# Optimization experiments

Hardware: AMD Instinct MI355X
Metric: run time of the kernel (lower is better)

## Reference

```python
import jax, jax.numpy as jnp
import numpy as np

NUM_CLASSES = 26
PERCENTILE = 95.0
BIG = jnp.float32(1e10)


def _erode(m):
    # scipy-style binary erosion with cross structuring element, border_value=0
    p = jnp.pad(m, 1, constant_values=False)
    return m & p[:-2, 1:-1] & p[2:, 1:-1] & p[1:-1, :-2] & p[1:-1, 2:]


def _boundary(m):
    return m & ~_erode(m)


def _edt(edge):
    # Exact Euclidean distance transform to nearest True pixel of `edge` [H, W].
    # Two-pass separable formulation (rows then columns), fully vectorized.
    H, W = edge.shape
    r = jnp.arange(H)
    rd2 = ((r[:, None] - r[None, :]) ** 2).astype(jnp.float32)  # [H, H']
    # g[i, j] = min over i' with edge[i', j] of (i - i')^2
    g = jnp.min(jnp.where(edge[None, :, :], rd2[:, :, None], BIG), axis=1)  # [H, W]
    c = jnp.arange(W)
    cd2 = ((c[:, None] - c[None, :]) ** 2).astype(jnp.float32)  # [W', W]
    # dt2[i, j] = min over j' of g[i, j'] + (j' - j)^2
    dt2 = jnp.min(g[:, :, None] + cd2[None, :, :], axis=1)  # [H, W]
    return jnp.sqrt(dt2)


def _pct95(dists, mask):
    # np.percentile(dists[mask], 95) with linear interpolation; nan if mask empty
    n = jnp.sum(mask)
    s = jnp.sort(jnp.where(mask, dists, jnp.inf))
    idx = (PERCENTILE / 100.0) * (n.astype(jnp.float32) - 1.0)
    idx = jnp.maximum(idx, 0.0)
    lo = jnp.floor(idx).astype(jnp.int32)
    hi = jnp.ceil(idx).astype(jnp.int32)
    vlo = s[lo]
    vhi = s[hi]
    val = vlo + (vhi - vlo) * (idx - jnp.floor(idx))
    return jnp.where(n > 0, val, jnp.nan)


def _hd_pair(pl, tl, c):
    # 95th-percentile symmetric Hausdorff between pred/target binary masks of class c
    pm = pl == c
    tm = tl == c
    pe = _boundary(pm)
    te = _boundary(tm)
    dt_t = _edt(te)  # distance to target boundary
    dt_p = _edt(pe)  # distance to pred boundary
    d_pt = _pct95(dt_t.ravel(), pe.ravel())  # pred-edge -> target-edge
    d_tp = _pct95(dt_p.ravel(), te.ravel())  # target-edge -> pred-edge
    return jnp.maximum(d_pt, d_tp)


def setup_inputs() -> dict:
    key = jax.random.key(0)
    k1, k2 = jax.random.split(key)
    predicted = jax.random.normal(k1, (2, NUM_CLASSES, 256, 256), dtype=jnp.float32)
    target = jax.random.normal(k2, (2, NUM_CLASSES, 256, 256), dtype=jnp.float32)
    return {"predicted": predicted, "target": target}


def reference(predicted, target):
    probs = jax.nn.softmax(predicted, axis=1)
    pl = jnp.argmax(probs, axis=1)   # [B, H, W]
    tl = jnp.argmax(target, axis=1)  # [B, H, W]

    def per_class(c):
        hd = jax.vmap(lambda p, t: _hd_pair(p, t, c))(pl, tl)  # [B]
        present = jnp.any(tl == c, axis=(1, 2))                # [B]
        return hd, present

    hds, pres = jax.lax.map(per_class, jnp.arange(NUM_CLASSES))  # [C, B]
    presf = pres.astype(jnp.float32)
    num = jnp.sum(jnp.where(pres, hds, 0.0), axis=0)  # [B]
    den = jnp.sum(presf, axis=0)                      # [B]
    batch_means = num / jnp.maximum(den, 1.0)
    valid = den > 0
    total = jnp.sum(jnp.where(valid, batch_means, 0.0)) / jnp.maximum(
        jnp.sum(valid.astype(jnp.float32)), 1.0)
    return jnp.where(jnp.any(valid), total, jnp.inf)
```

## Files before the change

kernel.cpp:

```cpp
#include <hip/hip_runtime.h>
#include <math.h>

#define HW 65536
#define NC 26
#define NB 2

#define PL_OFF    0
#define TL_OFF    131072
#define CNT_OFF   262144
#define RES_OFF   263424
#define BMP_OFF   264192
#define LISTP_OFF 1116160
#define LISTT_OFF 7931904
#define MINP_OFF  14747648
#define MINT_OFF  28379136

__global__ void k_labels(const float4* __restrict__ pred, const float4* __restrict__ targ,
                         uchar4* __restrict__ pl, uchar4* __restrict__ tl,
                         unsigned int* __restrict__ cnt) {
    int tid = threadIdx.x;
    if (blockIdx.x == 0) {
        for (int i = tid; i < 320; i += 128) cnt[i] = 0;
    }
    int idx = blockIdx.x * 128 + tid;
    if (idx >= (NB * HW / 4)) return;
    int b = idx >> 14, q = idx & 16383;
    const float4* p = pred + ((size_t)b * NC << 14) + q;
    const float4* t = targ + ((size_t)b * NC << 14) + q;
    float4 bp = p[0]; uchar4 ap = {0, 0, 0, 0};
    float4 bt = t[0]; uchar4 at = {0, 0, 0, 0};
#pragma unroll
    for (int c = 1; c < NC; ++c) {
        float4 vp = p[(size_t)c << 14];
        if (vp.x > bp.x) { bp.x = vp.x; ap.x = (unsigned char)c; }
        if (vp.y > bp.y) { bp.y = vp.y; ap.y = (unsigned char)c; }
        if (vp.z > bp.z) { bp.z = vp.z; ap.z = (unsigned char)c; }
        if (vp.w > bp.w) { bp.w = vp.w; ap.w = (unsigned char)c; }
        float4 vt = t[(size_t)c << 14];
        if (vt.x > bt.x) { bt.x = vt.x; at.x = (unsigned char)c; }
        if (vt.y > bt.y) { bt.y = vt.y; at.y = (unsigned char)c; }
        if (vt.z > bt.z) { bt.z = vt.z; at.z = (unsigned char)c; }
        if (vt.w > bt.w) { bt.w = vt.w; at.w = (unsigned char)c; }
    }
    pl[idx] = ap;
    tl[idx] = at;
}

__device__ __forceinline__ bool is_boundary(const unsigned char* __restrict__ L, int hw, int c) {
    int y = hw >> 8, x = hw & 255;
    if (y == 0 || y == 255 || x == 0 || x == 255) return true;
    return (int)L[hw - 256] != c || (int)L[hw + 256] != c ||
           (int)L[hw - 1]   != c || (int)L[hw + 1]   != c;
}

__global__ void k_rowbm(const unsigned char* __restrict__ pl,
                        const unsigned char* __restrict__ tl,
                        unsigned int* __restrict__ bmp,
                        unsigned int* __restrict__ cnt,
                        unsigned short* __restrict__ listP,
                        unsigned short* __restrict__ listT) {
    __shared__ unsigned bm[52][8];
    __shared__ unsigned lh[52];
    __shared__ unsigned lb[52];
    int tid = threadIdx.x;
    int b = blockIdx.x >> 8, y = blockIdx.x & 255;
    for (int i = tid; i < 416; i += 256) ((unsigned*)bm)[i] = 0;
    if (tid < 52) lh[tid] = 0;
    __syncthreads();
    const unsigned char* Lp = pl + (b << 16);
    const unsigned char* Lt = tl + (b << 16);
    int hw = (y << 8) | tid;
    int cp = Lp[hw];
    int ct = Lt[hw];
    bool bnp = is_boundary(Lp, hw, cp);
    bool bnt = is_boundary(Lt, hw, ct);
    unsigned rp = 0, rt = 0;
    if (bnp) {
        atomicOr(&bm[cp][tid >> 5], 1u << (tid & 31));
        rp = atomicAdd(&lh[cp], 1u);
    }
    if (bnt) {
        atomicOr(&bm[26 + ct][tid >> 5], 1u << (tid & 31));
        rt = atomicAdd(&lh[26 + ct], 1u);
    }
    __syncthreads();
    for (int i = tid; i < 416; i += 256) {
        int idx = i >> 3, w = i & 7;
        int m = idx < 26 ? 0 : 1;
        int c = idx < 26 ? idx : idx - 26;
        bmp[(((m * 52 + b * 26 + c) << 8) | y) * 8 + w] = bm[idx][w];
    }
    if (tid < 26)
        lb[tid] = lh[tid] ? atomicAdd(&cnt[208 + b * 26 + tid], lh[tid]) : 0u;
    else if (tid < 52)
        lb[tid] = lh[tid] ? atomicAdd(&cnt[260 + b * 26 + (tid - 26)], lh[tid]) : 0u;
    __syncthreads();
    if (bnp) listP[((unsigned)(b * 26 + cp) << 16) + lb[cp] + rp] = (unsigned short)hw;
    if (bnt) listT[((unsigned)(b * 26 + ct) << 16) + lb[26 + ct] + rt] = (unsigned short)hw;
}

__device__ __forceinline__ int row_dx(const unsigned* sb, const unsigned* rmw,
                                      int r, int xw, int xb) {
    unsigned RM = rmw[r];
    if (!RM) return 999;
    const unsigned* row = sb + r * 9;
    int dxmin = 999;
    unsigned m = row[xw];
    unsigned le = 0xFFFFFFFFu >> (31 - xb);
    unsigned lm = m & le;
    if (lm) dxmin = xb - 31 + __clz(lm);
    unsigned rmm = m & ~le;
    if (rmm) dxmin = min(dxmin, (__ffs(rmm) - 1) - xb);
    unsigned Lm = RM & ((1u << xw) - 1u);
    if (Lm) {
        int w1 = 31 - __clz(Lm);
        unsigned m1 = row[w1];
        dxmin = min(dxmin, xb + ((xw - w1) << 5) - (31 - __clz(m1)));
    }
    unsigned Rm = RM >> (xw + 1);
    if (Rm) {
        int w2 = xw + __ffs(Rm);
        unsigned m2 = row[w2];
        dxmin = min(dxmin, ((w2 - xw) << 5) + (__ffs(m2) - 1) - xb);
    }
    return dxmin;
}

__global__ __launch_bounds__(256) void k_ring(
        const unsigned int* __restrict__ cnt,
        const unsigned int* __restrict__ bmp,
        const unsigned short* __restrict__ listP,
        const unsigned short* __restrict__ listT,
        float* __restrict__ minP, float* __restrict__ minT) {
    int pair = blockIdx.y;
    int dir = blockIdx.z;
    unsigned ns = cnt[(dir ? 260 : 208) + pair];
    unsigned i0 = blockIdx.x * 256u;
    if (i0 >= ns) return;
    unsigned nt = cnt[(dir ? 208 : 260) + pair];
    if (nt == 0) return;
    const unsigned short* src = (dir ? listT : listP) + ((unsigned)pair << 16);
    float* outv = (dir ? minT : minP) + ((unsigned)pair << 16);

    __shared__ unsigned sb[256 * 9];
    __shared__ unsigned rmw[256];
    int tid = threadIdx.x;
    {
        const uint4* g4 = (const uint4*)(bmp + ((unsigned)((dir ? 0 : 52) + pair) << 11));
#pragma unroll
        for (int t = 0; t < 2; ++t) {
            int idx = tid + t * 256;
            uint4 v = g4[idx];
            unsigned* row = sb + (idx >> 1) * 9 + ((idx & 1) << 2);
            row[0] = v.x; row[1] = v.y; row[2] = v.z; row[3] = v.w;
        }
    }
    __syncthreads();
    {
        const unsigned* row = sb + tid * 9;
        unsigned rm = 0;
#pragma unroll
        for (int w = 0; w < 8; ++w) rm |= (row[w] ? 1u : 0u) << w;
        rmw[tid] = rm;
    }
    __syncthreads();

    unsigned stride = gridDim.x * 256u;
    for (unsigned ib = i0; ib < ns; ib += stride) {
        unsigned i = ib + tid;
        if (i >= ns) continue;
        unsigned h = src[i];
        int x = (int)(h & 255u);
        int sy = (int)(h >> 8);
        int xw = x >> 5, xb = x & 31;
        int best = 0x40000000;
        for (int k = 0; k < 256; ++k) {
            int k2 = k * k;
            if (k2 >= best) break;
            int ra = sy - k, rb = sy + k;
            if (ra < 0 && rb > 255) break;
            if (ra >= 0) {
                int dx = row_dx(sb, rmw, ra, xw, xb);
                if (dx < 999) best = min(best, k2 + dx * dx);
            }
            if (k && rb < 256) {
                int dx = row_dx(sb, rmw, rb, xw, xb);
                if (dx < 999) best = min(best, k2 + dx * dx);
            }
        }
        outv[i] = (float)best;
    }
}

__global__ void k_select(const unsigned int* __restrict__ cnt,
                         const float* __restrict__ minP, const float* __restrict__ minT,
                         float* __restrict__ res) {
    int pair = blockIdx.x;
    int dir = blockIdx.y;
    unsigned ns = cnt[(dir ? 260 : 208) + pair];
    unsigned nt = cnt[(dir ? 208 : 260) + pair];
    const float* vals = (dir ? minT : minP) + ((unsigned)pair << 16);
    int tid = threadIdx.x;

    if (ns == 0) { if (tid == 0) res[pair * 2 + dir] = nanf(""); return; }
    if (nt == 0) { if (tid == 0) res[pair * 2 + dir] = sqrtf(1e10f); return; }

    __shared__ unsigned hist[1024];
    __shared__ unsigned f1[128], f2[128];
    __shared__ int s_binlo, s_binhi, s_below_lo, s_below_hi;

    for (int i = tid; i < 1024; i += 256) hist[i] = 0;
    __syncthreads();
    for (unsigned i = tid; i < ns; i += 256) {
        int v = (int)vals[i];
        atomicAdd(&hist[v >> 7], 1u);
    }
    __syncthreads();

    float idxf = 0.95f * ((float)ns - 1.0f);
    if (idxf < 0.f) idxf = 0.f;
    int klo = (int)floorf(idxf);
    int khi = (int)ceilf(idxf);

    if (tid == 0) {
        unsigned cum = 0;
        int binlo = -1, binhi = -1, below_lo = 0, below_hi = 0;
        for (int bkt = 0; bkt < 1024; ++bkt) {
            unsigned h = hist[bkt];
            if (binlo < 0 && cum + h > (unsigned)klo) { binlo = bkt; below_lo = (int)cum; }
            if (binhi < 0 && cum + h > (unsigned)khi) { binhi = bkt; below_hi = (int)cum; }
            cum += h;
            if (binhi >= 0) break;
        }
        s_binlo = binlo; s_binhi = binhi; s_below_lo = below_lo; s_below_hi = below_hi;
    }
    __syncthreads();
    if (tid < 128) { f1[tid] = 0; f2[tid] = 0; }
    __syncthreads();
    int binlo = s_binlo, binhi = s_binhi;
    for (unsigned i = tid; i < ns; i += 256) {
        int v = (int)vals[i];
        int bkt = v >> 7;
        if (bkt == binlo) atomicAdd(&f1[v & 127], 1u);
        if (bkt == binhi && binhi != binlo) atomicAdd(&f2[v & 127], 1u);
    }
    __syncthreads();
    if (tid == 0) {
        int rlo = klo - s_below_lo;
        unsigned cum = 0; int d2lo = binlo << 7, d2hi = binhi << 7;
        for (int j = 0; j < 128; ++j) {
            cum += f1[j];
            if ((int)cum > rlo) { d2lo = (binlo << 7) + j; break; }
        }
        if (binhi == binlo) {
            int rhi = khi - s_below_lo;
            cum = 0;
            for (int j = 0; j < 128; ++j) {
                cum += f1[j];
                if ((int)cum > rhi) { d2hi = (binlo << 7) + j; break; }
            }
        } else {
            int rhi = khi - s_below_hi;
            cum = 0;
            for (int j = 0; j < 128; ++j) {
                cum += f2[j];
                if ((int)cum > rhi) { d2hi = (binhi << 7) + j; break; }
            }
        }
        float vlo = sqrtf((float)d2lo);
        float vhi = sqrtf((float)d2hi);
        float frac = idxf - floorf(idxf);
        res[pair * 2 + dir] = vlo + (vhi - vlo) * frac;
    }
}

__global__ void k_final(const unsigned int* __restrict__ cnt, const float* __restrict__ res,
                        float* __restrict__ out) {
    if (threadIdx.x != 0 || blockIdx.x != 0) return;
    float total = 0.f, nvalid = 0.f;
    bool anyv = false;
    for (int b = 0; b < NB; ++b) {
        float num = 0.f, den = 0.f;
        for (int c = 0; c < NC; ++c) {
            int pair = b * NC + c;
            bool present = cnt[260 + pair] > 0;
            float dpt = res[pair * 2];
            float dtp = res[pair * 2 + 1];
            float hd;
            if (isnan(dpt) || isnan(dtp)) hd = nanf("");
            else hd = fmaxf(dpt, dtp);
            if (present) { num += hd; den += 1.f; }
        }
        float bm = num / fmaxf(den, 1.f);
        if (den > 0.f) { total += bm; nvalid += 1.f; anyv = true; }
    }
    out[0] = anyv ? (total / fmaxf(nvalid, 1.f)) : INFINITY;
}

extern "C" void kernel_launch(void* const* d_in, const int* in_sizes, int n_in,
                              void* d_out, int out_size, void* d_ws, size_t ws_size,
                              hipStream_t stream) {
    const float* pred = (const float*)d_in[0];
    const float* targ = (const float*)d_in[1];
    float* out = (float*)d_out;
    char* ws = (char*)d_ws;

    unsigned char* pl = (unsigned char*)(ws + PL_OFF);
    unsigned char* tl = (unsigned char*)(ws + TL_OFF);
    unsigned int* cnt = (unsigned int*)(ws + CNT_OFF);
    float* res = (float*)(ws + RES_OFF);
    unsigned int* bmp = (unsigned int*)(ws + BMP_OFF);
    unsigned short* listP = (unsigned short*)(ws + LISTP_OFF);
    unsigned short* listT = (unsigned short*)(ws + LISTT_OFF);
    float* minP = (float*)(ws + MINP_OFF);
    float* minT = (float*)(ws + MINT_OFF);

    k_labels<<<256, 128, 0, stream>>>((const float4*)pred, (const float4*)targ,
                                      (uchar4*)pl, (uchar4*)tl, cnt);
    k_rowbm<<<512, 256, 0, stream>>>(pl, tl, bmp, cnt, listP, listT);
    k_ring<<<dim3(12, 52, 2), 256, 0, stream>>>(cnt, bmp, listP, listT, minP, minT);
    k_select<<<dim3(52, 2), 256, 0, stream>>>(cnt, minP, minT, res);
    k_final<<<1, 64, 0, stream>>>(cnt, res, out);
}
```

Measured before the change: 46.66 us.

## Fuse select and final reduction via last-block atomic; shrink ring blocks

Merges the percentile-select and final-averaging kernels into one, where the last block to finish (detected by an atomic counter) computes the final mean. This removes one kernel launch. It also halves the ring kernel's block size while doubling its grid, and stores each row's word-occupancy mask in the padding slot of the shared bitmap row instead of a separate array. The final-reduction path relies on the counter at cnt[313] being zeroed each call by the label kernel and on atomics to make other blocks' writes visible.

Result: slower. 79.24 us (+69.8%).

```diff
diff --git a/kernel.cpp b/kernel.cpp
--- a/kernel.cpp
+++ b/kernel.cpp
@@ -99,11 +99,10 @@
     if (bnt) listT[((unsigned)(b * 26 + ct) << 16) + lb[26 + ct] + rt] = (unsigned short)hw;
 }
 
-__device__ __forceinline__ int row_dx(const unsigned* sb, const unsigned* rmw,
-                                      int r, int xw, int xb) {
-    unsigned RM = rmw[r];
+__device__ __forceinline__ int row_dx(const unsigned* sb, int r, int xw, int xb) {
+    const unsigned* row = sb + r * 9;
+    unsigned RM = row[8];
     if (!RM) return 999;
-    const unsigned* row = sb + r * 9;
     int dxmin = 999;
     unsigned m = row[xw];
     unsigned le = 0xFFFFFFFFu >> (31 - xb);
@@ -126,7 +125,7 @@
     return dxmin;
 }
 
-__global__ __launch_bounds__(256) void k_ring(
+__global__ __launch_bounds__(128) void k_ring(
         const unsigned int* __restrict__ cnt,
         const unsigned int* __restrict__ bmp,
         const unsigned short* __restrict__ listP,
@@ -135,7 +134,7 @@
     int pair = blockIdx.y;
     int dir = blockIdx.z;
     unsigned ns = cnt[(dir ? 260 : 208) + pair];
-    unsigned i0 = blockIdx.x * 256u;
+    unsigned i0 = blockIdx.x * 128u;
     if (i0 >= ns) return;
     unsigned nt = cnt[(dir ? 208 : 260) + pair];
     if (nt == 0) return;
@@ -143,29 +142,28 @@
     float* outv = (dir ? minT : minP) + ((unsigned)pair << 16);
 
     __shared__ unsigned sb[256 * 9];
-    __shared__ unsigned rmw[256];
     int tid = threadIdx.x;
     {
         const uint4* g4 = (const uint4*)(bmp + ((unsigned)((dir ? 0 : 52) + pair) << 11));
 #pragma unroll
-        for (int t = 0; t < 2; ++t) {
-            int idx = tid + t * 256;
+        for (int t = 0; t < 4; ++t) {
+            int idx = tid + t * 128;
             uint4 v = g4[idx];
             unsigned* row = sb + (idx >> 1) * 9 + ((idx & 1) << 2);
             row[0] = v.x; row[1] = v.y; row[2] = v.z; row[3] = v.w;
         }
     }
     __syncthreads();
-    {
-        const unsigned* row = sb + tid * 9;
+    for (int r = tid; r < 256; r += 128) {
+        const unsigned* row = sb + r * 9;
         unsigned rm = 0;
 #pragma unroll
         for (int w = 0; w < 8; ++w) rm |= (row[w] ? 1u : 0u) << w;
-        rmw[tid] = rm;
-    }
-    __syncthreads();
-
-    unsigned stride = gridDim.x * 256u;
+        sb[r * 9 + 8] = rm;
+    }
+    __syncthreads();
+
+    unsigned stride = gridDim.x * 128u;
     for (unsigned ib = i0; ib < ns; ib += stride) {
         unsigned i = ib + tid;
         if (i >= ns) continue;
@@ -180,11 +178,11 @@
             int ra = sy - k, rb = sy + k;
             if (ra < 0 && rb > 255) break;
             if (ra >= 0) {
-                int dx = row_dx(sb, rmw, ra, xw, xb);
+                int dx = row_dx(sb, ra, xw, xb);
                 if (dx < 999) best = min(best, k2 + dx * dx);
             }
             if (k && rb < 256) {
-                int dx = row_dx(sb, rmw, rb, xw, xb);
+                int dx = row_dx(sb, rb, xw, xb);
                 if (dx < 999) best = min(best, k2 + dx * dx);
             }
         }
@@ -192,109 +190,118 @@
     }
 }
 
-__global__ void k_select(const unsigned int* __restrict__ cnt,
-                         const float* __restrict__ minP, const float* __restrict__ minT,
-                         float* __restrict__ res) {
+__global__ __launch_bounds__(256) void k_selfin(
+        unsigned int* cnt,
+        const float* __restrict__ minP, const float* __restrict__ minT,
+        float* res, float* __restrict__ out) {
     int pair = blockIdx.x;
     int dir = blockIdx.y;
+    int tid = threadIdx.x;
     unsigned ns = cnt[(dir ? 260 : 208) + pair];
     unsigned nt = cnt[(dir ? 208 : 260) + pair];
     const float* vals = (dir ? minT : minP) + ((unsigned)pair << 16);
-    int tid = threadIdx.x;
-
-    if (ns == 0) { if (tid == 0) res[pair * 2 + dir] = nanf(""); return; }
-    if (nt == 0) { if (tid == 0) res[pair * 2 + dir] = sqrtf(1e10f); return; }
 
     __shared__ unsigned hist[1024];
     __shared__ unsigned f1[128], f2[128];
     __shared__ int s_binlo, s_binhi, s_below_lo, s_below_hi;
-
-    for (int i = tid; i < 1024; i += 256) hist[i] = 0;
-    __syncthreads();
-    for (unsigned i = tid; i < ns; i += 256) {
-        int v = (int)vals[i];
-        atomicAdd(&hist[v >> 7], 1u);
-    }
-    __syncthreads();
-
-    float idxf = 0.95f * ((float)ns - 1.0f);
-    if (idxf < 0.f) idxf = 0.f;
-    int klo = (int)floorf(idxf);
-    int khi = (int)ceilf(idxf);
-
-    if (tid == 0) {
-        unsigned cum = 0;
-        int binlo = -1, binhi = -1, below_lo = 0, below_hi = 0;
-        for (int bkt = 0; bkt < 1024; ++bkt) {
-            unsigned h = hist[bkt];
-            if (binlo < 0 && cum + h > (unsigned)klo) { binlo = bkt; below_lo = (int)cum; }
-            if (binhi < 0 && cum + h > (unsigned)khi) { binhi = bkt; below_hi = (int)cum; }
-            cum += h;
-            if (binhi >= 0) break;
-        }
-        s_binlo = binlo; s_binhi = binhi; s_below_lo = below_lo; s_below_hi = below_hi;
-    }
-    __syncthreads();
-    if (tid < 128) { f1[tid] = 0; f2[tid] = 0; }
-    __syncthreads();
-    int binlo = s_binlo, binhi = s_binhi;
-    for (unsigned i = tid; i < ns; i += 256) {
-        int v = (int)vals[i];
-        int bkt = v >> 7;
-        if (bkt == binlo) atomicAdd(&f1[v & 127], 1u);
-        if (bkt == binhi && binhi != binlo) atomicAdd(&f2[v & 127], 1u);
-    }
-    __syncthreads();
-    if (tid == 0) {
-        int rlo = klo - s_below_lo;
-        unsigned cum = 0; int d2lo = binlo << 7, d2hi = binhi << 7;
-        for (int j = 0; j < 128; ++j) {
-            cum += f1[j];
-            if ((int)cum > rlo) { d2lo = (binlo << 7) + j; break; }
-        }
-        if (binhi == binlo) {
-            int rhi = khi - s_below_lo;
-            cum = 0;
+    __shared__ float s_result;
+
+    if (ns == 0) {
+        if (tid == 0) s_result = nanf("");
+    } else if (nt == 0) {
+        if (tid == 0) s_result = sqrtf(1e10f);
+    } else {
+        for (int i = tid; i < 1024; i += 256) hist[i] = 0;
+        if (tid < 128) { f1[tid] = 0; f2[tid] = 0; }
+        __syncthreads();
+        for (unsigned i = tid; i < ns; i += 256) {
+            int v = (int)vals[i];
+            atomicAdd(&hist[v >> 7], 1u);
+        }
+        __syncthreads();
+
+        float idxf = 0.95f * ((float)ns - 1.0f);
+        if (idxf < 0.f) idxf = 0.f;
+        int klo = (int)floorf(idxf);
+        int khi = (int)ceilf(idxf);
+
+        if (tid == 0) {
+            unsigned cum = 0;
+            int binlo = -1, binhi = -1, below_lo = 0, below_hi = 0;
+            for (int bkt = 0; bkt < 1024; ++bkt) {
+                unsigned h = hist[bkt];
+                if (binlo < 0 && cum + h > (unsigned)klo) { binlo = bkt; below_lo = (int)cum; }
+                if (binhi < 0 && cum + h > (unsigned)khi) { binhi = bkt; below_hi = (int)cum; }
+                cum += h;
+                if (binhi >= 0) break;
+            }
+            s_binlo = binlo; s_binhi = binhi; s_below_lo = below_lo; s_below_hi = below_hi;
+        }
+        __syncthreads();
+        int binlo = s_binlo, binhi = s_binhi;
+        for (unsigned i = tid; i < ns; i += 256) {
+            int v = (int)vals[i];
+            int bkt = v >> 7;
+            if (bkt == binlo) atomicAdd(&f1[v & 127], 1u);
+            if (bkt == binhi && binhi != binlo) atomicAdd(&f2[v & 127], 1u);
+        }
+        __syncthreads();
+        if (tid == 0) {
+            int rlo = klo - s_below_lo;
+            unsigned cum = 0; int d2lo = binlo << 7, d2hi = binhi << 7;
             for (int j = 0; j < 128; ++j) {
                 cum += f1[j];
-                if ((int)cum > rhi) { d2hi = (binlo << 7) + j; break; }
-            }
-        } else {
-            int rhi = khi - s_below_hi;
-            cum = 0;
-            for (int j = 0; j < 128; ++j) {
-                cum += f2[j];
-                if ((int)cum > rhi) { d2hi = (binhi << 7) + j; break; }
-            }
-        }
-        float vlo = sqrtf((float)d2lo);
-        float vhi = sqrtf((float)d2hi);
-        float frac = idxf - floorf(idxf);
-        res[pair * 2 + dir] = vlo + (vhi - vlo) * frac;
-    }
-}
-
-__global__ void k_final(const unsigned int* __restrict__ cnt, const float* __restrict__ res,
-                        float* __restrict__ out) {
-    if (threadIdx.x != 0 || blockIdx.x != 0) return;
-    float total = 0.f, nvalid = 0.f;
-    bool anyv = false;
-    for (int b = 0; b < NB; ++b) {
-        float num = 0.f, den = 0.f;
-        for (int c = 0; c < NC; ++c) {
-            int pair = b * NC + c;
-            bool present = cnt[260 + pair] > 0;
-            float dpt = res[pair * 2];
-            float dtp = res[pair * 2 + 1];
-            float hd;
-            if (isnan(dpt) || isnan(dtp)) hd = nanf("");
-            else hd = fmaxf(dpt, dtp);
-            if (present) { num += hd; den += 1.f; }
-        }
-        float bm = num / fmaxf(den, 1.f);
-        if (den > 0.f) { total += bm; nvalid += 1.f; anyv = true; }
-    }
-    out[0] = anyv ? (total / fmaxf(nvalid, 1.f)) : INFINITY;
+                if ((int)cum > rlo) { d2lo = (binlo << 7) + j; break; }
+            }
+            if (binhi == binlo) {
+                int rhi = khi - s_below_lo;
+                cum = 0;
+                for (int j = 0; j < 128; ++j) {
+                    cum += f1[j];
+                    if ((int)cum > rhi) { d2hi = (binlo << 7) + j; break; }
+                }
+            } else {
+                int rhi = khi - s_below_hi;
+                cum = 0;
+                for (int j = 0; j < 128; ++j) {
+                    cum += f2[j];
+                    if ((int)cum > rhi) { d2hi = (binhi << 7) + j; break; }
+                }
+            }
+            float vlo = sqrtf((float)d2lo);
+            float vhi = sqrtf((float)d2hi);
+            float frac = idxf - floorf(idxf);
+            s_result = vlo + (vhi - vlo) * frac;
+        }
+    }
+    __syncthreads();
+
+    if (tid == 0) {
+        float old = atomicExch(&res[(pair << 1) | dir], s_result);
+        asm volatile("" :: "v"(old));
+        unsigned t = atomicAdd(&cnt[313], 1u);
+        if (t == 103u) {
+            float total = 0.f, nvalid = 0.f;
+            bool anyv = false;
+            for (int b = 0; b < NB; ++b) {
+                float num = 0.f, den = 0.f;
+#pragma unroll
+                for (int c = 0; c < NC; ++c) {
+                    int pr = b * NC + c;
+                    bool present = cnt[260 + pr] > 0;
+                    float dpt = atomicAdd(&res[pr * 2], 0.0f);
+                    float dtp = atomicAdd(&res[pr * 2 + 1], 0.0f);
+                    float hd;
+                    if (isnan(dpt) || isnan(dtp)) hd = nanf("");
+                    else hd = fmaxf(dpt, dtp);
+                    if (present) { num += hd; den += 1.f; }
+                }
+                float bm = num / fmaxf(den, 1.f);
+                if (den > 0.f) { total += bm; nvalid += 1.f; anyv = true; }
+            }
+            out[0] = anyv ? (total / fmaxf(nvalid, 1.f)) : INFINITY;
+        }
+    }
 }
 
 extern "C" void kernel_launch(void* const* d_in, const int* in_sizes, int n_in,
@@ -318,7 +325,6 @@
     k_labels<<<256, 128, 0, stream>>>((const float4*)pred, (const float4*)targ,
                                       (uchar4*)pl, (uchar4*)tl, cnt);
     k_rowbm<<<512, 256, 0, stream>>>(pl, tl, bmp, cnt, listP, listT);
-    k_ring<<<dim3(12, 52, 2), 256, 0, stream>>>(cnt, bmp, listP, listT, minP, minT);
-    k_select<<<dim3(52, 2), 256, 0, stream>>>(cnt, minP, minT, res);
-    k_final<<<1, 64, 0, stream>>>(cnt, res, out);
-}
+    k_ring<<<dim3(24, 52, 2), 128, 0, stream>>>(cnt, bmp, listP, listT, minP, minT);
+    k_selfin<<<dim3(52, 2), 256, 0, stream>>>(cnt, minP, minT, res, out);
+}
```
